# Optimization experiments

Hardware: AMD Instinct MI355X
Metric: run time of the kernel (lower is better)

The kernel has to match this reference:

```python
import jax, jax.numpy as jnp
import numpy as np

D = 512      # embedding_dimension
L1 = 1024    # english sentence length
L2 = 1024    # french sentence length
V1 = 32000   # english vocab
V2 = 32000   # french vocab
NNEG = 8192  # negative samples
SCALE = 0.05 # param init scale (keeps exp() stable)


def setup_inputs() -> dict:
    key = jax.random.key(0)
    ks = jax.random.split(key, 32)
    def n(k, shape):
        return jax.random.normal(k, shape, dtype=jnp.float32) * SCALE
    inp = {}
    inp["en"] = jax.random.randint(ks[0], (L1,), 0, V1)
    inp["fr"] = jax.random.randint(ks[1], (L2,), 0, V2)
    inp["en_neg"] = jax.random.randint(ks[2], (NNEG,), 0, V1)
    inp["fr_neg"] = jax.random.randint(ks[3], (NNEG,), 0, V2)
    # input embeddings
    inp["emb"] = n(ks[4], (V1, D))
    # 3-layer BiLSTM, hidden=D per direction; layer0 in=D, layers 1-2 in=2D
    inp["Wih0"] = n(ks[5], (2, 4 * D, D)); inp["Whh0"] = n(ks[6], (2, 4 * D, D)); inp["b0"] = n(ks[7], (2, 4 * D))
    inp["Wih1"] = n(ks[8], (2, 4 * D, 2 * D)); inp["Whh1"] = n(ks[9], (2, 4 * D, D)); inp["b1"] = n(ks[10], (2, 4 * D))
    inp["Wih2"] = n(ks[11], (2, 4 * D, 2 * D)); inp["Whh2"] = n(ks[12], (2, 4 * D, D)); inp["b2"] = n(ks[13], (2, 4 * D))
    # inference nets (mu and sigma, 2-layer each)
    inp["Wmu1"] = n(ks[14], (D, D)); inp["bmu1"] = n(ks[15], (D,))
    inp["Wmu2"] = n(ks[16], (D, D)); inp["bmu2"] = n(ks[17], (D,))
    inp["Ws1"] = n(ks[18], (D, D)); inp["bs1"] = n(ks[19], (D,))
    inp["Ws2"] = n(ks[20], (D, D)); inp["bs2"] = n(ks[21], (D,))
    # softmax-approximation embedding tables
    inp["E_en"] = n(ks[22], (V1, D))
    inp["E_fr"] = n(ks[23], (V2, D))
    # reparameterization noise (epsilon.sample() per token, made explicit)
    inp["eps"] = jax.random.normal(ks[24], (L1, D), dtype=jnp.float32)
    return inp


def _lstm_bidir(xs, Wih, Whh, b):
    # xs: (L, in); Wih: (2, 4D, in); Whh: (2, 4D, D); b: (2, 4D)
    def run(d, reverse):
        Wi, Wh, bb = Wih[d], Whh[d], b[d]
        def step(carry, x):
            h, c = carry
            g = Wi @ x + Wh @ h + bb
            i, f, gg, o = jnp.split(g, 4)
            i = jax.nn.sigmoid(i); f = jax.nn.sigmoid(f)
            gg = jnp.tanh(gg); o = jax.nn.sigmoid(o)
            c = f * c + i * gg
            h = o * jnp.tanh(c)
            return (h, c), h
        init = (jnp.zeros((Wh.shape[1],), xs.dtype), jnp.zeros((Wh.shape[1],), xs.dtype))
        _, hs = jax.lax.scan(step, init, xs, reverse=reverse)
        return hs
    return run(0, False), run(1, True)  # each (L, D)


def reference(en, fr, en_neg, fr_neg, emb,
              Wih0, Whh0, b0, Wih1, Whh1, b1, Wih2, Whh2, b2,
              Wmu1, bmu1, Wmu2, bmu2, Ws1, bs1, Ws2, bs2,
              E_en, E_fr, eps):
    x = emb[en]                                   # (L1, D)
    hf, hb = _lstm_bidir(x, Wih0, Whh0, b0)
    hf, hb = _lstm_bidir(jnp.concatenate([hf, hb], -1), Wih1, Whh1, b1)
    hf, hb = _lstm_bidir(jnp.concatenate([hf, hb], -1), Wih2, Whh2, b2)
    h = hf + hb                                   # fwd+bwd hidden sum (intermediate[0][0]+intermediate[0][1])
    mu = jax.nn.relu(h @ Wmu1.T + bmu1) @ Wmu2.T + bmu2
    sigma = jax.nn.softplus(jax.nn.relu(h @ Ws1.T + bs1) @ Ws2.T + bs2)
    z = mu + eps * sigma                          # reparameterized sample (L1, D)
    # closed-form KL( N(mu, diag(sigma^2)) || N(0, I) ), summed over tokens
    kl = 0.5 * jnp.sum(sigma ** 2 + mu ** 2 - 1.0 - 2.0 * jnp.log(sigma))
    # english negative-sampling softmax approximation, summed over tokens
    pos = jnp.exp(jnp.sum(z * E_en[en], axis=-1))            # (L1,)
    neg = jnp.sum(jnp.exp(z @ E_en[en_neg].T), axis=-1)      # (L1,)
    sum_x = jnp.sum(pos / (pos + neg))
    # alignment scoring: every french token vs every english latent z
    s = jnp.exp(z @ E_fr[fr].T)                               # (L1, L2)
    negf = jnp.sum(jnp.exp(z @ E_fr[fr_neg].T), -1, keepdims=True)  # (L1, 1)
    p = s / (s + negf)                                        # (L1, L2)
    sum_y = jnp.sum(p) / L1                                   # uniform-alignment marginal
    return -(sum_x + sum_y - kl)


if __name__ == "__main__":
    out = reference(**setup_inputs())
    print(out)
```

## Files before the change

kernel.cpp:

```cpp
#include <hip/hip_runtime.h>
#include <hip/hip_bf16.h>


template<bool GATHER, bool RELU, int EPI>
__global__ __launch_bounds__(256) void gemm_nt(
    const float* __restrict__ A, const float* __restrict__ B,
    const float* __restrict__ bias, const int* __restrict__ idx,
    float* __restrict__ C, const float* __restrict__ negf,
    float* __restrict__ outsum, int M, int N, int K)
{
    __shared__ float As[16][68];
    __shared__ float Bs[16][68];
    __shared__ float wsum[4];

    const int tid = threadIdx.x;
    const int bm = blockIdx.x, bn = blockIdx.y;
    const int tx = tid & 15, ty = tid >> 4;
    const int lr = tid >> 2;
    const int lk = (tid & 3) * 4;

    const long arow = (long)bm * 64 + lr;
    const int  brow = bn * 64 + lr;
    const long bsrc = GATHER ? (long)idx[brow] : (long)brow;
    const float* Ap = A + arow * K + lk;
    const float* Bp = B + bsrc * K + lk;

    float acc[4][4] = {};

    for (int k0 = 0; k0 < K; k0 += 16) {
        float4 av = *(const float4*)(Ap + k0);
        float4 bv = *(const float4*)(Bp + k0);
        __syncthreads();
        As[lk + 0][lr] = av.x; As[lk + 1][lr] = av.y;
        As[lk + 2][lr] = av.z; As[lk + 3][lr] = av.w;
        Bs[lk + 0][lr] = bv.x; Bs[lk + 1][lr] = bv.y;
        Bs[lk + 2][lr] = bv.z; Bs[lk + 3][lr] = bv.w;
        __syncthreads();
#pragma unroll
        for (int k = 0; k < 16; ++k) {
            float4 a = *(const float4*)&As[k][ty * 4];
            float4 b = *(const float4*)&Bs[k][tx * 4];
            float ar[4] = {a.x, a.y, a.z, a.w};
            float br[4] = {b.x, b.y, b.z, b.w};
#pragma unroll
            for (int i = 0; i < 4; ++i)
#pragma unroll
                for (int j = 0; j < 4; ++j)
                    acc[i][j] += ar[i] * br[j];
        }
    }

    const int row0 = bm * 64 + ty * 4, col0 = bn * 64 + tx * 4;

    if (EPI == 0) {
#pragma unroll
        for (int i = 0; i < 4; ++i) {
            float4 v;
            float vv[4];
#pragma unroll
            for (int j = 0; j < 4; ++j) {
                float x = acc[i][j];
                if (bias) x += bias[col0 + j];
                if (RELU) x = x > 0.f ? x : 0.f;
                vv[j] = x;
            }
            v.x = vv[0]; v.y = vv[1]; v.z = vv[2]; v.w = vv[3];
            *(float4*)&C[(long)(row0 + i) * N + col0] = v;
        }
    } else if (EPI == 1) {
#pragma unroll
        for (int i = 0; i < 4; ++i) {
            float s = expf(acc[i][0]) + expf(acc[i][1]) +
                      expf(acc[i][2]) + expf(acc[i][3]);
            s += __shfl_xor(s, 1); s += __shfl_xor(s, 2);
            s += __shfl_xor(s, 4); s += __shfl_xor(s, 8);
            if (tx == 0) atomicAdd(&C[row0 + i], s);
        }
    } else {
        float t = 0.f;
#pragma unroll
        for (int i = 0; i < 4; ++i) {
            float nf = negf[row0 + i];
#pragma unroll
            for (int j = 0; j < 4; ++j) {
                float e = expf(acc[i][j]);
                t += e / (e + nf);
            }
        }
#pragma unroll
        for (int o = 1; o < 64; o <<= 1) t += __shfl_xor(t, o);
        if ((tid & 63) == 0) wsum[tid >> 6] = t;
        __syncthreads();
        if (tid == 0) atomicAdd(outsum, wsum[0] + wsum[1] + wsum[2] + wsum[3]);
    }
}

__global__ __launch_bounds__(256, 1) void lstm_scan(
    const float* __restrict__ Xf, const float* __restrict__ Xb,
    const float* __restrict__ Whh,
    float* __restrict__ out,
    unsigned long long* __restrict__ hbuf)
{
    const int tid  = threadIdx.x;
    const int dir  = blockIdx.x >> 6;
    const int w    = blockIdx.x & 63;
    const int r    = tid >> 3;
    const int ck   = tid & 7;
    const int gate = r >> 3;
    const int jl   = r & 7;
    const int j    = w * 8 + jl;
    const int grow = gate * 512 + j;

    const float* Wrow = Whh + ((long)dir * 2048 + grow) * 512 + ck * 64;
    float4 wv[16];
#pragma unroll
    for (int q = 0; q < 16; ++q) wv[q] = *(const float4*)(Wrow + q * 4);

    const float* Xp = dir ? Xb : Xf;
    unsigned long long* myh = hbuf + dir * 1024;

    __shared__ float hs[512];
    __shared__ float ga[32];

    float c = 0.f;
    bool dead = false;

    for (int s = 0; s < 1024; ++s) {
        const int t = dir ? (1023 - s) : s;
        float xg = Xp[(long)t * 2048 + grow];

        unsigned long long* rb = myh + ((s + 1) & 1) * 512;
        unsigned long long v0, v1;
        unsigned it = 0;
        for (;;) {
            v0 = __hip_atomic_load(&rb[tid],       __ATOMIC_RELAXED, __HIP_MEMORY_SCOPE_AGENT);
            v1 = __hip_atomic_load(&rb[tid + 256], __ATOMIC_RELAXED, __HIP_MEMORY_SCOPE_AGENT);
            if (dead || ((int)(v0 >> 32) == s && (int)(v1 >> 32) == s)) break;
            if (++it > (1u << 20)) { dead = true; break; }
        }
        hs[tid]       = __uint_as_float((unsigned)v0);
        hs[tid + 256] = __uint_as_float((unsigned)v1);
        __syncthreads();

        float a0 = 0.f, a1 = 0.f, a2 = 0.f, a3 = 0.f;
#pragma unroll
        for (int q = 0; q < 4; ++q) {
            const float4* hp4 = (const float4*)&hs[ck * 64 + q * 16];
            float4 h0 = hp4[0], h1 = hp4[1], h2 = hp4[2], h3 = hp4[3];
            float4 w0 = wv[4*q], w1 = wv[4*q+1], w2 = wv[4*q+2], w3 = wv[4*q+3];
            a0 += w0.x*h0.x + w0.y*h0.y + w0.z*h0.z + w0.w*h0.w;
            a1 += w1.x*h1.x + w1.y*h1.y + w1.z*h1.z + w1.w*h1.w;
            a2 += w2.x*h2.x + w2.y*h2.y + w2.z*h2.z + w2.w*h2.w;
            a3 += w3.x*h3.x + w3.y*h3.y + w3.z*h3.z + w3.w*h3.w;
        }
        float acc = (a0 + a1) + (a2 + a3);
        acc += __shfl_xor(acc, 1);
        acc += __shfl_xor(acc, 2);
        acc += __shfl_xor(acc, 4);
        if (ck == 0) ga[r] = acc + xg;
        __syncthreads();

        if (tid < 8) {
            float gi = ga[tid], gf = ga[8 + tid], gg = ga[16 + tid], go = ga[24 + tid];
            float i_ = 1.f / (1.f + expf(-gi));
            float f_ = 1.f / (1.f + expf(-gf));
            float g_ = tanhf(gg);
            float o_ = 1.f / (1.f + expf(-go));
            c = f_ * c + i_ * g_;
            float h = o_ * tanhf(c);
            unsigned long long pk = (unsigned long long)__float_as_uint(h)
                                  | ((unsigned long long)(unsigned)(s + 1) << 32);
            __hip_atomic_store(&myh[(s & 1) * 512 + w * 8 + tid], pk,
                               __ATOMIC_RELAXED, __HIP_MEMORY_SCOPE_AGENT);
            out[(long)t * 1024 + dir * 512 + w * 8 + tid] = h;
        }
    }
}

__global__ __launch_bounds__(128) void gather_emb(
    const int* __restrict__ en, const float* __restrict__ emb, float* __restrict__ x0)
{
    const int t = blockIdx.x;
    ((float4*)(x0 + (long)t * 512))[threadIdx.x] =
        ((const float4*)(emb + (long)en[t] * 512))[threadIdx.x];
}

__global__ __launch_bounds__(256) void add_h(
    const float* __restrict__ o2, float* __restrict__ h)
{
    const long i = (long)blockIdx.x * 256 + threadIdx.x;
    const long t = i >> 9, j = i & 511;
    h[i] = o2[t * 1024 + j] + o2[t * 1024 + 512 + j];
}

__global__ __launch_bounds__(256) void zkl_kernel(
    const float* __restrict__ mu, const float* __restrict__ sp,
    const float* __restrict__ eps, float* __restrict__ z, float* __restrict__ klsum)
{
    __shared__ float w4[4];
    const int i = blockIdx.x * 256 + threadIdx.x;
    float m = mu[i], x = sp[i];
    float sg = (x > 20.f) ? x : log1pf(expf(x));
    z[i] = m + eps[i] * sg;
    float kl = 0.5f * (sg * sg + m * m - 1.f) - logf(sg);
#pragma unroll
    for (int o = 1; o < 64; o <<= 1) kl += __shfl_xor(kl, o);
    if ((threadIdx.x & 63) == 0) w4[threadIdx.x >> 6] = kl;
    __syncthreads();
    if (threadIdx.x == 0) atomicAdd(klsum, w4[0] + w4[1] + w4[2] + w4[3]);
}

__global__ __launch_bounds__(64) void pos_kernel(
    const float* __restrict__ z, const float* __restrict__ E_en,
    const int* __restrict__ en, float* __restrict__ pos)
{
    const int t = blockIdx.x, lane = threadIdx.x;
    const float4* zr = (const float4*)(z + (long)t * 512);
    const float4* er = (const float4*)(E_en + (long)en[t] * 512);
    float s = 0.f;
#pragma unroll
    for (int q = 0; q < 2; ++q) {
        float4 a = zr[lane + q * 64], b = er[lane + q * 64];
        s += a.x * b.x + a.y * b.y + a.z * b.z + a.w * b.w;
    }
#pragma unroll
    for (int o = 1; o < 64; o <<= 1) s += __shfl_xor(s, o);
    if (lane == 0) pos[t] = expf(s);
}

__global__ __launch_bounds__(256) void finalize_kernel(
    const float* __restrict__ pos, const float* __restrict__ neg,
    const float* __restrict__ scal, float* __restrict__ out)
{
    __shared__ float w4[4];
    const int tid = threadIdx.x;
    float s = 0.f;
#pragma unroll
    for (int q = 0; q < 4; ++q) {
        int t = tid + q * 256;
        s += pos[t] / (pos[t] + neg[t]);
    }
#pragma unroll
    for (int o = 1; o < 64; o <<= 1) s += __shfl_xor(s, o);
    if ((tid & 63) == 0) w4[tid >> 6] = s;
    __syncthreads();
    if (tid == 0) {
        float sum_x = w4[0] + w4[1] + w4[2] + w4[3];
        out[0] = scal[0] - sum_x - scal[1] * (1.f / 1024.f);
    }
}

extern "C" void kernel_launch(void* const* d_in, const int* in_sizes, int n_in,
                              void* d_out, int out_size, void* d_ws, size_t ws_size,
                              hipStream_t stream)
{
    const int*   en     = (const int*)d_in[0];
    const int*   fr     = (const int*)d_in[1];
    const int*   en_neg = (const int*)d_in[2];
    const int*   fr_neg = (const int*)d_in[3];
    const float* emb    = (const float*)d_in[4];
    const float* Wih0   = (const float*)d_in[5];
    const float* Whh0   = (const float*)d_in[6];
    const float* b0     = (const float*)d_in[7];
    const float* Wih1   = (const float*)d_in[8];
    const float* Whh1   = (const float*)d_in[9];
    const float* b1     = (const float*)d_in[10];
    const float* Wih2   = (const float*)d_in[11];
    const float* Whh2   = (const float*)d_in[12];
    const float* b2     = (const float*)d_in[13];
    const float* Wmu1   = (const float*)d_in[14];
    const float* bmu1   = (const float*)d_in[15];
    const float* Wmu2   = (const float*)d_in[16];
    const float* bmu2   = (const float*)d_in[17];
    const float* Ws1    = (const float*)d_in[18];
    const float* bs1    = (const float*)d_in[19];
    const float* Ws2    = (const float*)d_in[20];
    const float* bs2    = (const float*)d_in[21];
    const float* E_en   = (const float*)d_in[22];
    const float* E_fr   = (const float*)d_in[23];
    const float* eps    = (const float*)d_in[24];
    float* out = (float*)d_out;

    float* w = (float*)d_ws;
    float* x0   = w;  w += 1024 * 512;
    float* bufA = w;  w += 1024 * 1024;
    float* bufB = w;  w += 1024 * 1024;
    float* Xf   = w;  w += 1024 * 2048;
    float* Xb   = w;  w += 1024 * 2048;
    float* h    = w;  w += 1024 * 512;
    float* tmp  = w;  w += 1024 * 512;
    float* mu   = w;  w += 1024 * 512;
    float* sp   = w;  w += 1024 * 512;
    float* z    = w;  w += 1024 * 512;
    float* pos  = w;  w += 1024;
    float* neg  = w;  w += 1024;
    float* negf = w;  w += 1024;
    unsigned long long* hbuf = (unsigned long long*)w; w += 4096;
    float* scal = w;  w += 2;

    hipMemsetAsync(neg, 0, 2048 * sizeof(float), stream);
    hipMemsetAsync(scal, 0, 2 * sizeof(float), stream);

    gather_emb<<<1024, 128, 0, stream>>>(en, emb, x0);

    gemm_nt<false, false, 0><<<dim3(16, 32), 256, 0, stream>>>(
        x0, Wih0,               b0,        nullptr, Xf, nullptr, nullptr, 1024, 2048, 512);
    gemm_nt<false, false, 0><<<dim3(16, 32), 256, 0, stream>>>(
        x0, Wih0 + 2048 * 512,  b0 + 2048, nullptr, Xb, nullptr, nullptr, 1024, 2048, 512);
    hipMemsetAsync(hbuf, 0, 4096 * 8, stream);
    lstm_scan<<<128, 256, 0, stream>>>(Xf, Xb, Whh0, bufA, hbuf);

    gemm_nt<false, false, 0><<<dim3(16, 32), 256, 0, stream>>>(
        bufA, Wih1,               b1,        nullptr, Xf, nullptr, nullptr, 1024, 2048, 1024);
    gemm_nt<false, false, 0><<<dim3(16, 32), 256, 0, stream>>>(
        bufA, Wih1 + 2048 * 1024, b1 + 2048, nullptr, Xb, nullptr, nullptr, 1024, 2048, 1024);
    hipMemsetAsync(hbuf, 0, 4096 * 8, stream);
    lstm_scan<<<128, 256, 0, stream>>>(Xf, Xb, Whh1, bufB, hbuf);

    gemm_nt<false, false, 0><<<dim3(16, 32), 256, 0, stream>>>(
        bufB, Wih2,               b2,        nullptr, Xf, nullptr, nullptr, 1024, 2048, 1024);
    gemm_nt<false, false, 0><<<dim3(16, 32), 256, 0, stream>>>(
        bufB, Wih2 + 2048 * 1024, b2 + 2048, nullptr, Xb, nullptr, nullptr, 1024, 2048, 1024);
    hipMemsetAsync(hbuf, 0, 4096 * 8, stream);
    lstm_scan<<<128, 256, 0, stream>>>(Xf, Xb, Whh2, bufA, hbuf);

    add_h<<<2048, 256, 0, stream>>>(bufA, h);

    gemm_nt<false, true, 0><<<dim3(16, 8), 256, 0, stream>>>(
        h,   Wmu1, bmu1, nullptr, tmp, nullptr, nullptr, 1024, 512, 512);
    gemm_nt<false, false, 0><<<dim3(16, 8), 256, 0, stream>>>(
        tmp, Wmu2, bmu2, nullptr, mu,  nullptr, nullptr, 1024, 512, 512);
    gemm_nt<false, true, 0><<<dim3(16, 8), 256, 0, stream>>>(
        h,   Ws1,  bs1,  nullptr, tmp, nullptr, nullptr, 1024, 512, 512);
    gemm_nt<false, false, 0><<<dim3(16, 8), 256, 0, stream>>>(
        tmp, Ws2,  bs2,  nullptr, sp,  nullptr, nullptr, 1024, 512, 512);

    zkl_kernel<<<2048, 256, 0, stream>>>(mu, sp, eps, z, scal);

    pos_kernel<<<1024, 64, 0, stream>>>(z, E_en, en, pos);
    gemm_nt<true, false, 1><<<dim3(16, 128), 256, 0, stream>>>(
        z, E_en, nullptr, en_neg, neg,  nullptr, nullptr, 1024, 8192, 512);
    gemm_nt<true, false, 1><<<dim3(16, 128), 256, 0, stream>>>(
        z, E_fr, nullptr, fr_neg, negf, nullptr, nullptr, 1024, 8192, 512);
    gemm_nt<true, false, 2><<<dim3(16, 16), 256, 0, stream>>>(
        z, E_fr, nullptr, fr,     nullptr, negf, scal + 1, 1024, 1024, 512);

    finalize_kernel<<<1, 256, 0, stream>>>(pos, neg, scal, out);
}
```

Before: 8.352 ms.

## Split LSTM scan over 256 blocks with recurrent weights in LDS

The persistent LSTM recurrence kernel now uses 256 blocks (128 per direction), each owning 4 hidden units instead of 8. Each thread handles a 32-element slice of a weight row and keeps it in padded shared memory rather than registers. The gate nonlinearities switch to fast __expf-based sigmoid and tanh. The aim is to halve per-block dot-product work on the serial critical path and spread it across more CUs. The cost is twice as many blocks polling the global h buffer each step, more shared-memory traffic, and slightly lower-precision activations; all 256 blocks must be co-resident or the spin-wait can deadlock.

```diff
diff --git a/kernel.cpp b/kernel.cpp
--- a/kernel.cpp
+++ b/kernel.cpp
@@ -102,28 +102,35 @@
     unsigned long long* __restrict__ hbuf)
 {
     const int tid  = threadIdx.x;
-    const int dir  = blockIdx.x >> 6;
-    const int w    = blockIdx.x & 63;
-    const int r    = tid >> 3;
-    const int ck   = tid & 7;
-    const int gate = r >> 3;
-    const int jl   = r & 7;
-    const int j    = w * 8 + jl;
+    const int dir  = blockIdx.x >> 7;
+    const int w    = blockIdx.x & 127;
+    const int r    = tid >> 4;
+    const int ck   = tid & 15;
+    const int gate = r >> 2;
+    const int jl   = r & 3;
+    const int j    = w * 4 + jl;
     const int grow = gate * 512 + j;
 
-    const float* Wrow = Whh + ((long)dir * 2048 + grow) * 512 + ck * 64;
-    float4 wv[16];
-#pragma unroll
-    for (int q = 0; q < 16; ++q) wv[q] = *(const float4*)(Wrow + q * 4);
+    __shared__ float Wl[256 * 36];
+    __shared__ float hs[16 * 36];
+    __shared__ float ga[16];
+
+    {
+        const float4* Wrow = (const float4*)(Whh + ((long)dir * 2048 + grow) * 512 + ck * 32);
+        float4* wl4 = (float4*)Wl + tid * 9;
+#pragma unroll
+        for (int q = 0; q < 8; ++q) wl4[q] = Wrow[q];
+    }
+    __syncthreads();
 
     const float* Xp = dir ? Xb : Xf;
     unsigned long long* myh = hbuf + dir * 1024;
 
-    __shared__ float hs[512];
-    __shared__ float ga[32];
-
     float c = 0.f;
     bool dead = false;
+
+    const float4* wl4 = (const float4*)Wl + tid * 9;
+    const float4* hs4 = (const float4*)hs + ck * 9;
 
     for (int s = 0; s < 1024; ++s) {
         const int t = dir ? (1023 - s) : s;
@@ -138,41 +145,42 @@
             if (dead || ((int)(v0 >> 32) == s && (int)(v1 >> 32) == s)) break;
             if (++it > (1u << 20)) { dead = true; break; }
         }
-        hs[tid]       = __uint_as_float((unsigned)v0);
-        hs[tid + 256] = __uint_as_float((unsigned)v1);
-        __syncthreads();
-
-        float a0 = 0.f, a1 = 0.f, a2 = 0.f, a3 = 0.f;
-#pragma unroll
-        for (int q = 0; q < 4; ++q) {
-            const float4* hp4 = (const float4*)&hs[ck * 64 + q * 16];
-            float4 h0 = hp4[0], h1 = hp4[1], h2 = hp4[2], h3 = hp4[3];
-            float4 w0 = wv[4*q], w1 = wv[4*q+1], w2 = wv[4*q+2], w3 = wv[4*q+3];
+        hs[((tid) >> 5) * 36 + (tid & 31)]             = __uint_as_float((unsigned)v0);
+        hs[((tid + 256) >> 5) * 36 + (tid & 31)]       = __uint_as_float((unsigned)v1);
+        __syncthreads();
+
+        float a0 = 0.f, a1 = 0.f;
+#pragma unroll
+        for (int q = 0; q < 8; q += 2) {
+            float4 w0 = wl4[q],     h0 = hs4[q];
+            float4 w1 = wl4[q + 1], h1 = hs4[q + 1];
             a0 += w0.x*h0.x + w0.y*h0.y + w0.z*h0.z + w0.w*h0.w;
             a1 += w1.x*h1.x + w1.y*h1.y + w1.z*h1.z + w1.w*h1.w;
-            a2 += w2.x*h2.x + w2.y*h2.y + w2.z*h2.z + w2.w*h2.w;
-            a3 += w3.x*h3.x + w3.y*h3.y + w3.z*h3.z + w3.w*h3.w;
-        }
-        float acc = (a0 + a1) + (a2 + a3);
+        }
+        float acc = a0 + a1;
         acc += __shfl_xor(acc, 1);
         acc += __shfl_xor(acc, 2);
         acc += __shfl_xor(acc, 4);
+        acc += __shfl_xor(acc, 8);
         if (ck == 0) ga[r] = acc + xg;
         __syncthreads();
 
-        if (tid < 8) {
-            float gi = ga[tid], gf = ga[8 + tid], gg = ga[16 + tid], go = ga[24 + tid];
-            float i_ = 1.f / (1.f + expf(-gi));
-            float f_ = 1.f / (1.f + expf(-gf));
-            float g_ = tanhf(gg);
-            float o_ = 1.f / (1.f + expf(-go));
+        if (tid < 4) {
+            float gi = ga[tid], gf = ga[4 + tid], gg = ga[8 + tid], go = ga[12 + tid];
+            float i_ = 1.f / (1.f + __expf(-gi));
+            float f_ = 1.f / (1.f + __expf(-gf));
+            float eg = __expf(2.f * gg);
+            float g_ = (eg - 1.f) / (eg + 1.f);
+            float o_ = 1.f / (1.f + __expf(-go));
             c = f_ * c + i_ * g_;
-            float h = o_ * tanhf(c);
+            float ec = __expf(2.f * c);
+            float tc = (ec - 1.f) / (ec + 1.f);
+            float h = o_ * tc;
             unsigned long long pk = (unsigned long long)__float_as_uint(h)
                                   | ((unsigned long long)(unsigned)(s + 1) << 32);
-            __hip_atomic_store(&myh[(s & 1) * 512 + w * 8 + tid], pk,
+            __hip_atomic_store(&myh[(s & 1) * 512 + w * 4 + tid], pk,
                                __ATOMIC_RELAXED, __HIP_MEMORY_SCOPE_AGENT);
-            out[(long)t * 1024 + dir * 512 + w * 8 + tid] = h;
+            out[(long)t * 1024 + dir * 512 + w * 4 + tid] = h;
         }
     }
 }
@@ -308,21 +316,21 @@
     gemm_nt<false, false, 0><<<dim3(16, 32), 256, 0, stream>>>(
         x0, Wih0 + 2048 * 512,  b0 + 2048, nullptr, Xb, nullptr, nullptr, 1024, 2048, 512);
     hipMemsetAsync(hbuf, 0, 4096 * 8, stream);
-    lstm_scan<<<128, 256, 0, stream>>>(Xf, Xb, Whh0, bufA, hbuf);
+    lstm_scan<<<256, 256, 0, stream>>>(Xf, Xb, Whh0, bufA, hbuf);
 
     gemm_nt<false, false, 0><<<dim3(16, 32), 256, 0, stream>>>(
         bufA, Wih1,               b1,        nullptr, Xf, nullptr, nullptr, 1024, 2048, 1024);
     gemm_nt<false, false, 0><<<dim3(16, 32), 256, 0, stream>>>(
         bufA, Wih1 + 2048 * 1024, b1 + 2048, nullptr, Xb, nullptr, nullptr, 1024, 2048, 1024);
     hipMemsetAsync(hbuf, 0, 4096 * 8, stream);
-    lstm_scan<<<128, 256, 0, stream>>>(Xf, Xb, Whh1, bufB, hbuf);
+    lstm_scan<<<256, 256, 0, stream>>>(Xf, Xb, Whh1, bufB, hbuf);
 
     gemm_nt<false, false, 0><<<dim3(16, 32), 256, 0, stream>>>(
         bufB, Wih2,               b2,        nullptr, Xf, nullptr, nullptr, 1024, 2048, 1024);
     gemm_nt<false, false, 0><<<dim3(16, 32), 256, 0, stream>>>(
         bufB, Wih2 + 2048 * 1024, b2 + 2048, nullptr, Xb, nullptr, nullptr, 1024, 2048, 1024);
     hipMemsetAsync(hbuf, 0, 4096 * 8, stream);
-    lstm_scan<<<128, 256, 0, stream>>>(Xf, Xb, Whh2, bufA, hbuf);
+    lstm_scan<<<256, 256, 0, stream>>>(Xf, Xb, Whh2, bufA, hbuf);
 
     add_h<<<2048, 256, 0, stream>>>(bufA, h);
 
```

Measured after the change: 7.148 ms. -14.4%, faster.
